# Performance work log

Hardware: AMD Instinct MI355X
Metric: run time of the kernel (lower is better)

Reference implementation:

```python
import jax, jax.numpy as jnp
import numpy as np

NUM_CENTROIDS = 2048
EMA_DECAY = 0.99
GAMMA = 1.0
EPS = 1e-08


def setup_inputs() -> dict:
    key = jax.random.key(0)
    k1, k2 = jax.random.split(key)
    B, T, D = 32, 512, 512
    inputs = jax.random.normal(k1, (B, T, D), dtype=jnp.float32)
    # variance_scaling(0.1, 'fan_avg', 'normal') init for the codebook
    fan_avg = (NUM_CENTROIDS + D) / 2.0
    std = np.sqrt(0.1 / fan_avg).astype(np.float32)
    codebook = jax.random.normal(k2, (NUM_CENTROIDS, D), dtype=jnp.float32) * std
    cluster_counts = jnp.ones((NUM_CENTROIDS,), dtype=jnp.float32)
    return {"inputs": inputs, "codebook": codebook,
            "cluster_counts": cluster_counts, "train": 1}


def reference(inputs, codebook, cluster_counts, train):
    D = inputs.shape[-1]
    K = codebook.shape[0]
    flat = jnp.reshape(inputs, (-1, D))  # [N, D]

    # similarity of stop-gradient features to codebook rows: [N, K]
    features = jax.lax.stop_gradient(flat)
    similarity = jnp.einsum('nd,kd->nk', features, codebook)
    scores = jax.nn.softmax(similarity, axis=-1)
    nn_idx = jnp.argmax(scores, axis=-1)  # [N]

    # cluster counts = column sums of one-hot encodings -> scatter-add
    counts = jnp.zeros((K,), dtype=scores.dtype).at[nn_idx].add(1.0)
    if train:
        new_counts = EMA_DECAY * cluster_counts + (1.0 - EMA_DECAY) * counts
    else:
        new_counts = cluster_counts

    # one_hot @ codebook == gather of codebook rows
    quantized = codebook[nn_idx]  # [N, D]
    quantized = quantized - jnp.mean(quantized, axis=-1, keepdims=True)
    quantized = quantized / jnp.linalg.norm(quantized, axis=-1, keepdims=True)
    quantized = jnp.reshape(quantized, inputs.shape)

    # entropy-based quantization loss (scalar), broadcast to [..., K]
    h_clust = -jnp.mean(jnp.sum(scores * jnp.log2(scores + EPS), axis=-1))
    diversity = jnp.mean(scores, axis=0)
    h_diversity = -jnp.sum(diversity * jnp.log2(diversity + EPS))
    loss = h_clust - GAMMA * h_diversity
    quantization_loss = jnp.full(inputs.shape[:-1] + (K,), loss)

    # straight-through estimator
    quantized = inputs + jax.lax.stop_gradient(quantized - inputs)

    nn_idx_out = jnp.reshape(nn_idx, inputs.shape[:-1])[None]  # [1, B, T]
    codebook_values = jax.lax.stop_gradient(codebook)[None]     # [1, K, D]
    return (quantized, quantization_loss, nn_idx_out, codebook_values, new_counts)
```

## Files before the change

### kernel.cpp

```cpp
#include <hip/hip_runtime.h>
#include <cstddef>
#include <cmath>

#define NROWS 16384
#define DIM   512
#define KC    2048

#define Q_OFF    0ul
#define LOSS_OFF 8388608ul
#define NN_OFF   41943040ul
#define CB_OFF   41959424ul
#define CNT_OFF  43008000ul

#define ENT_OFF  4194304ul

#define FLAG_CAP 4096
#define FLAG_TAU 3e-5f

#define WS_LOSS   0
#define WS_CNT    4
#define WS_NFLAG  3076
#define WS_FLAGS  3080
#define WS_DIVLOG 15376

typedef __attribute__((ext_vector_type(8))) short short8;
typedef __attribute__((ext_vector_type(4))) float f32x4;

__device__ __forceinline__ short hi1(float f) {
    return (short)(__float_as_uint(f) >> 16);
}
__device__ __forceinline__ short lo1(float f) {
    unsigned int u = __float_as_uint(f);
    float l = f - __uint_as_float(u & 0xffff0000u);
    return (short)(__float_as_uint(l) >> 16);
}
__device__ __forceinline__ short8 hi8(float4 a, float4 b) {
    short8 r;
    r[0]=hi1(a.x); r[1]=hi1(a.y); r[2]=hi1(a.z); r[3]=hi1(a.w);
    r[4]=hi1(b.x); r[5]=hi1(b.y); r[6]=hi1(b.z); r[7]=hi1(b.w);
    return r;
}
__device__ __forceinline__ short8 lo8(float4 a, float4 b) {
    short8 r;
    r[0]=lo1(a.x); r[1]=lo1(a.y); r[2]=lo1(a.z); r[3]=lo1(a.w);
    r[4]=lo1(b.x); r[5]=lo1(b.y); r[6]=lo1(b.z); r[7]=lo1(b.w);
    return r;
}

__global__ __launch_bounds__(256) void convsplit(const float* __restrict__ x,
                                                 const float* __restrict__ cb,
                                                 ushort* __restrict__ ah,
                                                 ushort* __restrict__ al,
                                                 ushort* __restrict__ bh,
                                                 ushort* __restrict__ bl,
                                                 int* __restrict__ ws) {
    if (blockIdx.x == 0) {
        for (int j = threadIdx.x + WS_CNT; j < WS_CNT + 2048; j += 256) ws[j] = 0;
        if (threadIdx.x == 0) ws[WS_NFLAG] = 0;
    }
    size_t i = (size_t)blockIdx.x * 256 + threadIdx.x;
    const float* src; ushort* dh; ushort* dl; size_t off;
    if (i < 1048576ul) {
        src = x;  dh = ah; dl = al; off = i * 8;
    } else {
        src = cb; dh = bh; dl = bl; off = (i - 1048576ul) * 8;
    }
    float4 a = *(const float4*)(src + off);
    float4 b = *(const float4*)(src + off + 4);
    *(short8*)(dh + off) = hi8(a, b);
    *(short8*)(dl + off) = lo8(a, b);
}

__global__ __launch_bounds__(256, 3) void gemm_mfma(const ushort* __restrict__ Ah,
                                                    const ushort* __restrict__ Al,
                                                    const ushort* __restrict__ Bh,
                                                    const ushort* __restrict__ Bl,
                                                    float* __restrict__ C) {
    __shared__ ushort smem[16384];
    const int t    = threadIdx.x;
    const int n0   = blockIdx.x * 128;
    const int m0   = blockIdx.y * 128;
    const int lane = t & 63, quad = lane >> 4, lr = lane & 15;
    const int w = t >> 6, wm = w >> 1, wn = w & 1;

    f32x4 acc[4][4] = {};

    const int srow = w * 32 + (lane >> 2);
    const int gc   = (((lane & 3) ^ ((lane >> 3) & 3)) << 3);

    const ushort* gAh0 = Ah + (size_t)(m0 + srow) * DIM + gc;
    const ushort* gAh1 = gAh0 + 16 * DIM;
    const ushort* gAl0 = Al + (size_t)(m0 + srow) * DIM + gc;
    const ushort* gAl1 = gAl0 + 16 * DIM;
    const ushort* gBh0 = Bh + (size_t)(n0 + srow) * DIM + gc;
    const ushort* gBh1 = gBh0 + 16 * DIM;
    const ushort* gBl0 = Bl + (size_t)(n0 + srow) * DIM + gc;
    const ushort* gBl1 = gBl0 + 16 * DIM;

    ushort* lAh = smem +     0 + w * 1024;
    ushort* lAl = smem +  4096 + w * 1024;
    ushort* lBh = smem +  8192 + w * 1024;
    ushort* lBl = smem + 12288 + w * 1024;

    const int swz = ((quad ^ ((lr >> 1) & 3)) << 3);
    const ushort* ra = smem +        (wm * 64 + lr) * 32 + swz;
    const ushort* rb = smem + 8192 + (wn * 64 + lr) * 32 + swz;

    #pragma unroll 1
    for (int kk = 0; kk < 16; ++kk) {
        const int k0 = kk * 32;
        #define GLD16(G, L)                                                         \
            __builtin_amdgcn_global_load_lds(                                       \
                (const __attribute__((address_space(1))) unsigned int*)(G),         \
                (__attribute__((address_space(3))) unsigned int*)(L), 16, 0, 0)
        GLD16(gAh0 + k0, lAh);
        GLD16(gAh1 + k0, lAh + 512);
        GLD16(gAl0 + k0, lAl);
        GLD16(gAl1 + k0, lAl + 512);
        GLD16(gBh0 + k0, lBh);
        GLD16(gBh1 + k0, lBh + 512);
        GLD16(gBl0 + k0, lBl);
        GLD16(gBl1 + k0, lBl + 512);
        #undef GLD16
        __syncthreads();

        short8 ah[4], al[4], bx[4];
        #pragma unroll
        for (int mt = 0; mt < 4; ++mt) ah[mt] = *(const short8*)(ra + mt * 512);
        #pragma unroll
        for (int nt = 0; nt < 4; ++nt) bx[nt] = *(const short8*)(rb + nt * 512);
        #pragma unroll
        for (int mt = 0; mt < 4; ++mt)
            #pragma unroll
            for (int nt = 0; nt < 4; ++nt)
                acc[mt][nt] = __builtin_amdgcn_mfma_f32_16x16x32_bf16(ah[mt], bx[nt], acc[mt][nt], 0, 0, 0);
        #pragma unroll
        for (int mt = 0; mt < 4; ++mt) al[mt] = *(const short8*)(ra + 4096 + mt * 512);
        #pragma unroll
        for (int mt = 0; mt < 4; ++mt)
            #pragma unroll
            for (int nt = 0; nt < 4; ++nt)
                acc[mt][nt] = __builtin_amdgcn_mfma_f32_16x16x32_bf16(al[mt], bx[nt], acc[mt][nt], 0, 0, 0);
        #pragma unroll
        for (int nt = 0; nt < 4; ++nt) bx[nt] = *(const short8*)(rb + 4096 + nt * 512);
        #pragma unroll
        for (int mt = 0; mt < 4; ++mt)
            #pragma unroll
            for (int nt = 0; nt < 4; ++nt)
                acc[mt][nt] = __builtin_amdgcn_mfma_f32_16x16x32_bf16(ah[mt], bx[nt], acc[mt][nt], 0, 0, 0);
        __syncthreads();
    }

    #pragma unroll
    for (int mt = 0; mt < 4; ++mt) {
        #pragma unroll
        for (int nt = 0; nt < 4; ++nt) {
            const int r0 = m0 + wm * 64 + mt * 16 + quad * 4;
            const int c0 = n0 + wn * 64 + nt * 16 + lr;
            #pragma unroll
            for (int j = 0; j < 4; ++j)
                C[(size_t)(r0 + j) * KC + c0] = acc[mt][nt][j];
        }
    }
}

__device__ __forceinline__ float block_reduce_sum(float v, volatile float* sf,
                                                  int lane, int w) {
    #pragma unroll
    for (int off = 32; off; off >>= 1) v += __shfl_xor(v, off, 64);
    if (lane == 0) sf[w] = v;
    __syncthreads();
    v = sf[0] + sf[1] + sf[2] + sf[3];
    __syncthreads();
    return v;
}

__global__ __launch_bounds__(256, 4) void rowpass(const float* __restrict__ sim,
                                                  float* __restrict__ nn,
                                                  float* __restrict__ divpart2,
                                                  int*   __restrict__ counts,
                                                  float* __restrict__ entpart,
                                                  int*   __restrict__ nflag,
                                                  int*   __restrict__ flags) {
    __shared__ float divp[KC];
    __shared__ float sent[4];
    const int t = threadIdx.x, lane = t & 63, w = t >> 6;
    const int b = blockIdx.x;
    const int row0 = b * 8 + w * 2;
    const int col0 = lane << 2;

    float4 dacc[8] = {};
    float ent_acc = 0.f;
    const float* base = sim + (size_t)row0 * KC + col0;

    #pragma unroll 1
    for (int rr = 0; rr < 2; ++rr) {
        float4 cur[8];
        const float* rp = base + (size_t)rr * KC;
        #pragma unroll
        for (int j = 0; j < 8; ++j) cur[j] = *(const float4*)(rp + 256 * j);

        float bv = -3.0e38f, rv = -3.0e38f;
        int   bi = 0x7fffffff, ri = 0x7fffffff;
        #pragma unroll
        for (int j = 0; j < 8; ++j) {
            #pragma unroll
            for (int c = 0; c < 4; ++c) {
                float v = (&cur[j].x)[c];
                int   i = col0 + c + 256 * j;
                if (v > bv || (v == bv && i < bi)) { rv = bv; ri = bi; bv = v; bi = i; }
                else if (v > rv || (v == rv && i < ri)) { rv = v; ri = i; }
            }
        }
        #pragma unroll
        for (int off = 32; off; off >>= 1) {
            float obv = __shfl_xor(bv, off, 64);
            int   obi = __shfl_xor(bi, off, 64);
            float orv = __shfl_xor(rv, off, 64);
            int   ori = __shfl_xor(ri, off, 64);
            bool ob = (obv > bv) || (obv == bv && obi < bi);
            float c1v = ob ? bv : obv;  int c1i = ob ? bi : obi;
            float c2v = ob ? orv : rv;  int c2i = ob ? ori : ri;
            bv = ob ? obv : bv;  bi = ob ? obi : bi;
            bool rb = (c1v > c2v) || (c1v == c2v && c1i < c2i);
            rv = rb ? c1v : c2v;  ri = rb ? c1i : c2i;
        }
        const float m = bv;

        float Z = 0.f, S = 0.f;
        #pragma unroll
        for (int j = 0; j < 8; ++j) {
            #pragma unroll
            for (int c = 0; c < 4; ++c) {
                float d = (&cur[j].x)[c] - m;
                float e = expf(d);
                Z += e; S += e * d;
                (&cur[j].x)[c] = e;
            }
        }
        #pragma unroll
        for (int off = 32; off; off >>= 1) {
            Z += __shfl_xor(Z, off, 64);
            S += __shfl_xor(S, off, 64);
        }
        const float inv = 1.0f / Z;
        #pragma unroll
        for (int j = 0; j < 8; ++j) {
            dacc[j].x += cur[j].x * inv; dacc[j].y += cur[j].y * inv;
            dacc[j].z += cur[j].z * inv; dacc[j].w += cur[j].w * inv;
        }

        if (lane == 0) {
            ent_acc += 1.4426950408889634f * (S * inv) - log2f(Z) + 2.9546393e-5f;
            atomicAdd(&counts[bi], 1);
            nn[row0 + rr] = (float)bi;
            if (bv - rv < FLAG_TAU) {
                int e = atomicAdd(nflag, 1);
                if (e < FLAG_CAP) {
                    flags[3*e] = row0 + rr; flags[3*e+1] = bi; flags[3*e+2] = ri;
                }
            }
        }
    }

    if (lane == 0) sent[w] = ent_acc;
    for (int ww = 0; ww < 4; ++ww) {
        if (w == ww) {
            #pragma unroll
            for (int j = 0; j < 8; ++j) {
                float4* p = (float4*)&divp[col0 + 256 * j];
                if (ww == 0) *p = dacc[j];
                else {
                    float4 v = *p;
                    v.x += dacc[j].x; v.y += dacc[j].y;
                    v.z += dacc[j].z; v.w += dacc[j].w;
                    *p = v;
                }
            }
        }
        __syncthreads();
    }
    float4* dst = (float4*)(divpart2 + (size_t)b * KC);
    dst[t]       = *(float4*)&divp[t * 4];
    dst[t + 256] = *(float4*)&divp[t * 4 + 1024];
    if (t == 0) entpart[b] = sent[0] + sent[1] + sent[2] + sent[3];
}

__global__ __launch_bounds__(256) void fixfin(const float* __restrict__ divpart2,
                                              float* __restrict__ part2,
                                              const float* __restrict__ A,
                                              const float* __restrict__ B,
                                              float* __restrict__ nn,
                                              int*   __restrict__ counts,
                                              const int* __restrict__ flags,
                                              const int* __restrict__ nflagp) {
    const int t = threadIdx.x;
    if (blockIdx.x < 128) {
        const int b = blockIdx.x;
        const float* dp = divpart2 + (size_t)b * 16 * KC;
        #pragma unroll
        for (int j = 0; j < 8; ++j) {
            int c = t + 256 * j;
            float s = 0.f;
            #pragma unroll
            for (int r = 0; r < 16; ++r) s += dp[(size_t)r * KC + c];
            part2[(size_t)b * KC + c] = s;
        }
    } else {
        __shared__ float sf[4];
        int nf = *nflagp; if (nf > FLAG_CAP) nf = FLAG_CAP;
        const int lane = t & 63, w = t >> 6;
        for (int e = blockIdx.x - 128; e < nf; e += 128) {
            const int row = flags[3*e], i1 = flags[3*e+1], i2 = flags[3*e+2];
            const float* ar = A + (size_t)row * DIM;
            const float* b1 = B + (size_t)i1 * DIM;
            const float* b2 = B + (size_t)i2 * DIM;
            float d1 = ar[t] * b1[t] + ar[t + 256] * b1[t + 256];
            float d2 = ar[t] * b2[t] + ar[t + 256] * b2[t + 256];
            d1 = block_reduce_sum(d1, sf, lane, w);
            d2 = block_reduce_sum(d2, sf, lane, w);
            if (t == 0 && (d2 > d1 || (d2 == d1 && i2 < i1))) {
                nn[row] = (float)i2;
                atomicSub(&counts[i1], 1);
                atomicAdd(&counts[i2], 1);
            }
            __syncthreads();
        }
    }
}

__global__ __launch_bounds__(256) void fin1b(const float* __restrict__ part2,
                                             float* __restrict__ divlog8) {
    __shared__ float sf[4];
    const int t = threadIdx.x, lane = t & 63, w = t >> 6;
    const int c = blockIdx.x * 256 + t;
    float s = 0.f;
    for (int r = 0; r < 128; ++r) s += part2[(size_t)r * KC + c];
    float d = s * (1.0f / 16384.0f);
    float v = d * log2f(d + 1e-8f);
    float S = block_reduce_sum(v, sf, lane, w);
    if (t == 0) divlog8[blockIdx.x] = S;
}

__global__ __launch_bounds__(256) void fin2(const float* __restrict__ entpart,
                                            const float* __restrict__ divlog8,
                                            float* __restrict__ lossp) {
    __shared__ float sf[4];
    const int t = threadIdx.x, lane = t & 63, w = t >> 6;
    float se = 0.f;
    #pragma unroll
    for (int k = 0; k < 8; ++k) se += entpart[t + 256 * k];
    float Se = block_reduce_sum(se, sf, lane, w);
    float Sd = block_reduce_sum((t < 8) ? divlog8[t] : 0.f, sf, lane, w);
    if (t == 0)
        lossp[0] = (float)(-(double)Se / 16384.0 + (double)Sd);
}

__global__ __launch_bounds__(256) void tail(const float* __restrict__ x,
                                            const float* __restrict__ cb,
                                            const float* __restrict__ oldc,
                                            const int*   __restrict__ counts,
                                            const float* __restrict__ lossp,
                                            const int*   __restrict__ train,
                                            const float* __restrict__ nn,
                                            float* __restrict__ out) {
    const int bb = blockIdx.x;
    const int t  = threadIdx.x;
    if (bb < 4096) {
        const int lane = t & 63;
        const int row  = (bb << 2) + (t >> 6);
        const int idx  = (int)nn[row];
        const float* c  = cb + (size_t)idx * DIM;
        const float* xr = x  + (size_t)row * DIM;

        float4 q0 = *(const float4*)(c + lane * 8);
        float4 q1 = *(const float4*)(c + lane * 8 + 4);

        float s = q0.x+q0.y+q0.z+q0.w + q1.x+q1.y+q1.z+q1.w;
        #pragma unroll
        for (int off = 32; off; off >>= 1) s += __shfl_xor(s, off, 64);
        const float mean = s * (1.0f / 512.0f);
        q0.x -= mean; q0.y -= mean; q0.z -= mean; q0.w -= mean;
        q1.x -= mean; q1.y -= mean; q1.z -= mean; q1.w -= mean;

        float ss = q0.x*q0.x+q0.y*q0.y+q0.z*q0.z+q0.w*q0.w
                 + q1.x*q1.x+q1.y*q1.y+q1.z*q1.z+q1.w*q1.w;
        #pragma unroll
        for (int off = 32; off; off >>= 1) ss += __shfl_xor(ss, off, 64);
        const float inv = 1.0f / sqrtf(ss);

        float4 x0 = *(const float4*)(xr + lane * 8);
        float4 x1 = *(const float4*)(xr + lane * 8 + 4);
        float4 o0, o1;
        o0.x = x0.x + (q0.x*inv - x0.x); o0.y = x0.y + (q0.y*inv - x0.y);
        o0.z = x0.z + (q0.z*inv - x0.z); o0.w = x0.w + (q0.w*inv - x0.w);
        o1.x = x1.x + (q1.x*inv - x1.x); o1.y = x1.y + (q1.y*inv - x1.y);
        o1.z = x1.z + (q1.z*inv - x1.z); o1.w = x1.w + (q1.w*inv - x1.w);
        *(float4*)(out + (size_t)row * DIM + lane * 8)     = o0;
        *(float4*)(out + (size_t)row * DIM + lane * 8 + 4) = o1;
    } else {
        const int bb2 = bb - 4096;
        if (bb2 < 8192) {
            const float l = lossp[0];
            const float4 v = make_float4(l, l, l, l);
            float4* lo = (float4*)(out + LOSS_OFF);
            size_t base4 = (size_t)bb2 * 1024 + t;
            lo[base4]       = v;
            lo[base4 + 256] = v;
            lo[base4 + 512] = v;
            lo[base4 + 768] = v;
        } else if (bb2 < 8192 + 1024) {
            size_t j = (size_t)(bb2 - 8192) * 256 + t;
            ((float4*)(out + CB_OFF))[j] = ((const float4*)cb)[j];
        } else {
            int k = (bb2 - 9216) * 256 + t;
            float nc = train[0] ? 0.99f * oldc[k] + 0.01f * (float)counts[k]
                                : oldc[k];
            out[CNT_OFF + k] = nc;
        }
    }
}

extern "C" void kernel_launch(void* const* d_in, const int* in_sizes, int n_in,
                              void* d_out, int out_size, void* d_ws, size_t ws_size,
                              hipStream_t stream) {
    const float* x     = (const float*)d_in[0];
    const float* cb    = (const float*)d_in[1];
    const float* oldc  = (const float*)d_in[2];
    const int*   train = (const int*)d_in[3];
    float* out = (float*)d_out;

    float* sim      = out + LOSS_OFF;
    float* divpart2 = out + Q_OFF;
    float* entpart  = out + Q_OFF + ENT_OFF;
    float* part2    = out + CB_OFF;
    float* nn       = out + NN_OFF;

    ushort* Ah = (ushort*)(out + Q_OFF);
    ushort* Al = Ah + 8388608ul;
    ushort* Bh = (ushort*)(out + CB_OFF);
    ushort* Bl = Bh + 1048576ul;

    float* lossp   = (float*)d_ws + WS_LOSS;
    int*   counts  = (int*)d_ws   + WS_CNT;
    int*   nflag   = (int*)d_ws   + WS_NFLAG;
    int*   flags   = (int*)d_ws   + WS_FLAGS;
    float* divlog8 = (float*)d_ws + WS_DIVLOG;

    convsplit<<<4608, 256, 0, stream>>>(x, cb, Ah, Al, Bh, Bl, (int*)d_ws);
    gemm_mfma<<<dim3(KC / 128, NROWS / 128), 256, 0, stream>>>(Ah, Al, Bh, Bl, sim);
    rowpass<<<2048, 256, 0, stream>>>(sim, nn, divpart2, counts, entpart, nflag, flags);
    fixfin<<<256, 256, 0, stream>>>(divpart2, part2, x, cb, nn, counts, flags, nflag);
    fin1b<<<8, 256, 0, stream>>>(part2, divlog8);
    fin2<<<1, 256, 0, stream>>>(entpart, divlog8, lossp);
    tail<<<4096 + 9224, 256, 0, stream>>>(x, cb, oldc, counts, lossp, train, nn, out);
}
```

Before: 365.9 us.

## Enlarge GEMM tile to 256x256 with double-buffered LDS and staged prefetch

The split-bf16 similarity GEMM now uses 512-thread blocks computing 256x256 output tiles, with 8 waves arranged 2x4. Each wave holds 8x4 MFMA accumulators. LDS is double-buffered so global-to-LDS loads for the next k-step are issued in three stages, interleaved with the three MFMA phases and gated by explicit vmcnt waits and barriers, with s_setprio raised around the MFMA bursts. The goal is better operand reuse per load and hiding global memory latency behind compute. In exchange, register pressure and LDS use (128 KB per block) go up, occupancy drops, and the hand-counted waitcnt logic is fragile.

Measured after the change: 354.1 us. -3.2%, faster.

```diff
diff --git a/kernel.cpp b/kernel.cpp
--- a/kernel.cpp
+++ b/kernel.cpp
@@ -71,19 +71,26 @@
     *(short8*)(dl + off) = lo8(a, b);
 }
 
-__global__ __launch_bounds__(256, 3) void gemm_mfma(const ushort* __restrict__ Ah,
+#define P_AH 0
+#define P_AL 8192
+#define P_BH 16384
+#define P_BL 24576
+#define BUFS 32768
+
+__global__ __launch_bounds__(512, 2) void gemm_mfma(const ushort* __restrict__ Ah,
                                                     const ushort* __restrict__ Al,
                                                     const ushort* __restrict__ Bh,
                                                     const ushort* __restrict__ Bl,
                                                     float* __restrict__ C) {
-    __shared__ ushort smem[16384];
+    __shared__ ushort smem[65536];
     const int t    = threadIdx.x;
-    const int n0   = blockIdx.x * 128;
-    const int m0   = blockIdx.y * 128;
+    const int n0   = blockIdx.x * 256;
+    const int m0   = blockIdx.y * 256;
     const int lane = t & 63, quad = lane >> 4, lr = lane & 15;
-    const int w = t >> 6, wm = w >> 1, wn = w & 1;
-
-    f32x4 acc[4][4] = {};
+    const int w = t >> 6, wm = w >> 2, wn = w & 3;
+    const int wb = w * 1024;
+
+    f32x4 acc[8][4] = {};
 
     const int srow = w * 32 + (lane >> 2);
     const int gc   = (((lane & 3) ^ ((lane >> 3) & 3)) << 3);
@@ -97,65 +104,136 @@
     const ushort* gBl0 = Bl + (size_t)(n0 + srow) * DIM + gc;
     const ushort* gBl1 = gBl0 + 16 * DIM;
 
-    ushort* lAh = smem +     0 + w * 1024;
-    ushort* lAl = smem +  4096 + w * 1024;
-    ushort* lBh = smem +  8192 + w * 1024;
-    ushort* lBl = smem + 12288 + w * 1024;
-
-    const int swz = ((quad ^ ((lr >> 1) & 3)) << 3);
-    const ushort* ra = smem +        (wm * 64 + lr) * 32 + swz;
-    const ushort* rb = smem + 8192 + (wn * 64 + lr) * 32 + swz;
+    const int swz   = ((quad ^ ((lr >> 1) & 3)) << 3);
+    const int raOff = (wm * 128 + lr) * 32 + swz;
+    const int rbOff = (wn * 64  + lr) * 32 + swz;
+
+    #define GLD16(G, LOFF)                                                          \
+        __builtin_amdgcn_global_load_lds(                                           \
+            (const __attribute__((address_space(1))) unsigned int*)(G),             \
+            (__attribute__((address_space(3))) unsigned int*)(smem + (LOFF)), 16, 0, 0)
+
+    GLD16(gAh0, P_AH + wb);
+    GLD16(gAh1, P_AH + wb + 512);
+    GLD16(gBh0, P_BH + wb);
+    GLD16(gBh1, P_BH + wb + 512);
+    GLD16(gAl0, P_AL + wb);
+    GLD16(gAl1, P_AL + wb + 512);
+    GLD16(gBl0, P_BL + wb);
+    GLD16(gBl1, P_BL + wb + 512);
+    asm volatile("s_waitcnt vmcnt(4)" ::: "memory");
+    __builtin_amdgcn_s_barrier();
+    __builtin_amdgcn_sched_barrier(0);
+
+    short8 ah[8], bb[4], al[8], bl[4];
 
     #pragma unroll 1
-    for (int kk = 0; kk < 16; ++kk) {
-        const int k0 = kk * 32;
-        #define GLD16(G, L)                                                         \
-            __builtin_amdgcn_global_load_lds(                                       \
-                (const __attribute__((address_space(1))) unsigned int*)(G),         \
-                (__attribute__((address_space(3))) unsigned int*)(L), 16, 0, 0)
-        GLD16(gAh0 + k0, lAh);
-        GLD16(gAh1 + k0, lAh + 512);
-        GLD16(gAl0 + k0, lAl);
-        GLD16(gAl1 + k0, lAl + 512);
-        GLD16(gBh0 + k0, lBh);
-        GLD16(gBh1 + k0, lBh + 512);
-        GLD16(gBl0 + k0, lBl);
-        GLD16(gBl1 + k0, lBl + 512);
-        #undef GLD16
-        __syncthreads();
-
-        short8 ah[4], al[4], bx[4];
-        #pragma unroll
-        for (int mt = 0; mt < 4; ++mt) ah[mt] = *(const short8*)(ra + mt * 512);
-        #pragma unroll
-        for (int nt = 0; nt < 4; ++nt) bx[nt] = *(const short8*)(rb + nt * 512);
-        #pragma unroll
-        for (int mt = 0; mt < 4; ++mt)
+    for (int kk = 0; kk < 15; ++kk) {
+        const int cb  = (kk & 1) * BUFS;
+        const int nb  = cb ^ BUFS;
+        const int k0n = (kk + 1) * 32;
+
+        #pragma unroll
+        for (int mt = 0; mt < 8; ++mt) ah[mt] = *(const short8*)(smem + cb + P_AH + raOff + mt * 512);
+        #pragma unroll
+        for (int nt = 0; nt < 4; ++nt) bb[nt] = *(const short8*)(smem + cb + P_BH + rbOff + nt * 512);
+        GLD16(gAh0 + k0n, nb + P_AH + wb);
+        GLD16(gAh1 + k0n, nb + P_AH + wb + 512);
+        GLD16(gBh0 + k0n, nb + P_BH + wb);
+        asm volatile("s_waitcnt vmcnt(5)" ::: "memory");
+        __builtin_amdgcn_s_barrier();
+        __builtin_amdgcn_sched_barrier(0);
+        __builtin_amdgcn_s_setprio(1);
+        #pragma unroll
+        for (int mt = 0; mt < 8; ++mt)
             #pragma unroll
             for (int nt = 0; nt < 4; ++nt)
-                acc[mt][nt] = __builtin_amdgcn_mfma_f32_16x16x32_bf16(ah[mt], bx[nt], acc[mt][nt], 0, 0, 0);
-        #pragma unroll
-        for (int mt = 0; mt < 4; ++mt) al[mt] = *(const short8*)(ra + 4096 + mt * 512);
-        #pragma unroll
-        for (int mt = 0; mt < 4; ++mt)
+                acc[mt][nt] = __builtin_amdgcn_mfma_f32_16x16x32_bf16(ah[mt], bb[nt], acc[mt][nt], 0, 0, 0);
+        __builtin_amdgcn_s_setprio(0);
+        __builtin_amdgcn_s_barrier();
+        __builtin_amdgcn_sched_barrier(0);
+
+        #pragma unroll
+        for (int mt = 0; mt < 8; ++mt) al[mt] = *(const short8*)(smem + cb + P_AL + raOff + mt * 512);
+        GLD16(gBh1 + k0n, nb + P_BH + wb + 512);
+        GLD16(gAl0 + k0n, nb + P_AL + wb);
+        GLD16(gAl1 + k0n, nb + P_AL + wb + 512);
+        asm volatile("s_waitcnt vmcnt(6)" ::: "memory");
+        __builtin_amdgcn_s_barrier();
+        __builtin_amdgcn_sched_barrier(0);
+        __builtin_amdgcn_s_setprio(1);
+        #pragma unroll
+        for (int mt = 0; mt < 8; ++mt)
             #pragma unroll
             for (int nt = 0; nt < 4; ++nt)
-                acc[mt][nt] = __builtin_amdgcn_mfma_f32_16x16x32_bf16(al[mt], bx[nt], acc[mt][nt], 0, 0, 0);
-        #pragma unroll
-        for (int nt = 0; nt < 4; ++nt) bx[nt] = *(const short8*)(rb + 4096 + nt * 512);
-        #pragma unroll
-        for (int mt = 0; mt < 4; ++mt)
+                acc[mt][nt] = __builtin_amdgcn_mfma_f32_16x16x32_bf16(al[mt], bb[nt], acc[mt][nt], 0, 0, 0);
+        __builtin_amdgcn_s_setprio(0);
+        __builtin_amdgcn_s_barrier();
+        __builtin_amdgcn_sched_barrier(0);
+
+        #pragma unroll
+        for (int nt = 0; nt < 4; ++nt) bl[nt] = *(const short8*)(smem + cb + P_BL + rbOff + nt * 512);
+        GLD16(gBl0 + k0n, nb + P_BL + wb);
+        GLD16(gBl1 + k0n, nb + P_BL + wb + 512);
+        asm volatile("s_waitcnt vmcnt(4)" ::: "memory");
+        __builtin_amdgcn_s_barrier();
+        __builtin_amdgcn_sched_barrier(0);
+        __builtin_amdgcn_s_setprio(1);
+        #pragma unroll
+        for (int mt = 0; mt < 8; ++mt)
             #pragma unroll
             for (int nt = 0; nt < 4; ++nt)
-                acc[mt][nt] = __builtin_amdgcn_mfma_f32_16x16x32_bf16(ah[mt], bx[nt], acc[mt][nt], 0, 0, 0);
-        __syncthreads();
-    }
+                acc[mt][nt] = __builtin_amdgcn_mfma_f32_16x16x32_bf16(ah[mt], bl[nt], acc[mt][nt], 0, 0, 0);
+        __builtin_amdgcn_s_setprio(0);
+        __builtin_amdgcn_s_barrier();
+        __builtin_amdgcn_sched_barrier(0);
+    }
+
+    {
+        const int cb = BUFS;
+        #pragma unroll
+        for (int mt = 0; mt < 8; ++mt) ah[mt] = *(const short8*)(smem + cb + P_AH + raOff + mt * 512);
+        #pragma unroll
+        for (int nt = 0; nt < 4; ++nt) bb[nt] = *(const short8*)(smem + cb + P_BH + rbOff + nt * 512);
+        asm volatile("s_waitcnt vmcnt(2)" ::: "memory");
+        __builtin_amdgcn_s_barrier();
+        __builtin_amdgcn_sched_barrier(0);
+        #pragma unroll
+        for (int mt = 0; mt < 8; ++mt)
+            #pragma unroll
+            for (int nt = 0; nt < 4; ++nt)
+                acc[mt][nt] = __builtin_amdgcn_mfma_f32_16x16x32_bf16(ah[mt], bb[nt], acc[mt][nt], 0, 0, 0);
+        __builtin_amdgcn_s_barrier();
+        __builtin_amdgcn_sched_barrier(0);
+
+        #pragma unroll
+        for (int mt = 0; mt < 8; ++mt) al[mt] = *(const short8*)(smem + cb + P_AL + raOff + mt * 512);
+        asm volatile("s_waitcnt vmcnt(0)" ::: "memory");
+        __builtin_amdgcn_s_barrier();
+        __builtin_amdgcn_sched_barrier(0);
+        #pragma unroll
+        for (int mt = 0; mt < 8; ++mt)
+            #pragma unroll
+            for (int nt = 0; nt < 4; ++nt)
+                acc[mt][nt] = __builtin_amdgcn_mfma_f32_16x16x32_bf16(al[mt], bb[nt], acc[mt][nt], 0, 0, 0);
+        __builtin_amdgcn_s_barrier();
+        __builtin_amdgcn_sched_barrier(0);
+
+        #pragma unroll
+        for (int nt = 0; nt < 4; ++nt) bl[nt] = *(const short8*)(smem + cb + P_BL + rbOff + nt * 512);
+        #pragma unroll
+        for (int mt = 0; mt < 8; ++mt)
+            #pragma unroll
+            for (int nt = 0; nt < 4; ++nt)
+                acc[mt][nt] = __builtin_amdgcn_mfma_f32_16x16x32_bf16(ah[mt], bl[nt], acc[mt][nt], 0, 0, 0);
+    }
+    #undef GLD16
 
     #pragma unroll
-    for (int mt = 0; mt < 4; ++mt) {
+    for (int mt = 0; mt < 8; ++mt) {
         #pragma unroll
         for (int nt = 0; nt < 4; ++nt) {
-            const int r0 = m0 + wm * 64 + mt * 16 + quad * 4;
+            const int r0 = m0 + wm * 128 + mt * 16 + quad * 4;
             const int c0 = n0 + wn * 64 + nt * 16 + lr;
             #pragma unroll
             for (int j = 0; j < 4; ++j)
@@ -448,7 +526,7 @@
     float* divlog8 = (float*)d_ws + WS_DIVLOG;
 
     convsplit<<<4608, 256, 0, stream>>>(x, cb, Ah, Al, Bh, Bl, (int*)d_ws);
-    gemm_mfma<<<dim3(KC / 128, NROWS / 128), 256, 0, stream>>>(Ah, Al, Bh, Bl, sim);
+    gemm_mfma<<<dim3(KC / 256, NROWS / 256), 512, 0, stream>>>(Ah, Al, Bh, Bl, sim);
     rowpass<<<2048, 256, 0, stream>>>(sim, nn, divpart2, counts, entpart, nflag, flags);
     fixfin<<<256, 256, 0, stream>>>(divpart2, part2, x, cb, nn, counts, flags, nflag);
     fin1b<<<8, 256, 0, stream>>>(part2, divlog8);
```
